# Kernel tuning notes

Hardware: AMD Instinct MI355X
Metric: run time of the kernel (lower is better)

Reference implementation:

```python
import jax, jax.numpy as jnp
import numpy as np

OT_REG = 0.1
OT_ITERS = 10
LN_EPS = 1e-5


def layernorm(x, g, b):
    m = jnp.mean(x, axis=-1, keepdims=True)
    v = jnp.mean((x - m) ** 2, axis=-1, keepdims=True)
    return (x - m) * jax.lax.rsqrt(v + LN_EPS) * g + b


def sinkhorn(C, epsilon, iters):
    # standard Sinkhorn: kernel exp(C/eps), alternate row/col normalization
    Q = jnp.exp(C / epsilon)  # [Na,B,La,Lb]
    def body(_, Q):
        Q = Q / jnp.sum(Q, axis=-1, keepdims=True)
        Q = Q / jnp.sum(Q, axis=-2, keepdims=True)
        return Q
    return jax.lax.fori_loop(0, iters, body, Q)


def setup_inputs() -> dict:
    key = jax.random.key(0)
    ks = jax.random.split(key, 16)
    Na, La, B, Lb, Din, H = 32, 32, 64, 32, 768, 768
    s = 0.02
    return {
        "entity_cls": jax.random.normal(ks[0], (Na, Din), jnp.float32),
        "entity_tokens": jax.random.normal(ks[1], (Na, La, Din), jnp.float32),
        "mention_cls": jax.random.normal(ks[2], (B, Din), jnp.float32),
        "mention_tokens": jax.random.normal(ks[3], (B, Lb, Din), jnp.float32),
        "Wq": jax.random.normal(ks[4], (Din, H), jnp.float32) * s,
        "bq": jnp.zeros((H,), jnp.float32),
        "Wk": jax.random.normal(ks[5], (Din, H), jnp.float32) * s,
        "bk": jnp.zeros((H,), jnp.float32),
        "Wv": jax.random.normal(ks[6], (Din, H), jnp.float32) * s,
        "bv": jnp.zeros((H,), jnp.float32),
        "ln1_g": jnp.ones((H,), jnp.float32),
        "ln1_b": jnp.zeros((H,), jnp.float32),
        "Wcls": jax.random.normal(ks[7], (Din, H), jnp.float32) * s,
        "bcls": jnp.zeros((H,), jnp.float32),
        "Wsp": jax.random.normal(ks[8], (H, 1), jnp.float32) * s,
        "bsp": jnp.zeros((1,), jnp.float32),
        "ln2_g": jnp.ones((H,), jnp.float32),
        "ln2_b": jnp.zeros((H,), jnp.float32),
    }


def reference(entity_cls, entity_tokens, mention_cls, mention_tokens,
              Wq, bq, Wk, bk, Wv, bv, ln1_g, ln1_b,
              Wcls, bcls, Wsp, bsp, ln2_g, ln2_b):
    # projections
    q = entity_tokens @ Wq + bq      # [Na,La,H]
    k = mention_tokens @ Wk + bk     # [B,Lb,H]
    v = mention_tokens @ Wv + bv     # [B,Lb,H]

    # cross-batch cosine similarity: [Na,B,La,Lb]
    qn = q / jnp.maximum(jnp.linalg.norm(q, axis=-1, keepdims=True), 1e-8)
    kn = k / jnp.maximum(jnp.linalg.norm(k, axis=-1, keepdims=True), 1e-8)
    C = jnp.einsum('aid,bjd->abij', qn, kn)

    # Sinkhorn on detached cost (torch uses C.detach())
    T = sinkhorn(jax.lax.stop_gradient(C), OT_REG, OT_ITERS)
    # F.normalize(dim=-1): L2 normalize last dim
    T = T / jnp.maximum(jnp.linalg.norm(T, axis=-1, keepdims=True), 1e-12)

    # attention + residual + layernorm: [Na,B,La,H]
    attended = jnp.einsum('abij,bjd->abid', T, v) + q[:, None, :, :]
    attended = layernorm(attended, ln1_g, ln1_b)

    # softpool over token dim (-2)
    w = jax.nn.softmax(attended @ Wsp + bsp, axis=-2)   # [Na,B,La,1]
    pooled = jnp.sum(attended * w, axis=-2)             # [Na,B,H]
    context = layernorm(pooled, ln2_g, ln2_b)

    # matching scores
    ecls = entity_cls @ Wcls + bcls                     # [Na,H]
    g2l = jnp.sum(ecls[:, None, :] * context, axis=-1)  # [Na,B]
    g2l = g2l.T                                         # [B,Na]
    g2g = mention_cls @ entity_cls.T                    # [B,Na]
    return (g2l + g2g) * 0.5
```

## Files before the change

### kernel.cpp

```cpp
#include <hip/hip_runtime.h>
#include <math.h>


typedef __attribute__((ext_vector_type(8))) short bfrag8;
typedef __attribute__((ext_vector_type(4))) float f32x4;

__device__ __forceinline__ unsigned short f2bf(float x) {
  union { float f; unsigned u; } v; v.f = x;
  unsigned r = v.u + 0x7fffu + ((v.u >> 16) & 1u);
  return (unsigned short)(r >> 16);
}

__global__ __launch_bounds__(256) void prep_kernel(
    const float* __restrict__ a0, const float* __restrict__ a1, const float* __restrict__ a2,
    unsigned short* __restrict__ o0, unsigned short* __restrict__ o1, unsigned short* __restrict__ o2,
    float* __restrict__ nrm,
    const float* __restrict__ W0, const float* __restrict__ W1,
    const float* __restrict__ W2, const float* __restrict__ W3,
    unsigned short* __restrict__ T0, unsigned short* __restrict__ T1,
    unsigned short* __restrict__ T2, unsigned short* __restrict__ T3) {
  __shared__ float t[32][33];
  int bx = blockIdx.x;
  if (bx < 2331) {
    if (bx < 2328) {
      const float* in; unsigned short* out; int i, n4;
      if (bx < 768)       { in = a0; out = o0; i = bx * 256 + threadIdx.x;          n4 = 196608; }
      else if (bx < 2304) { in = a1; out = o1; i = (bx - 768) * 256 + threadIdx.x;  n4 = 393216; }
      else                { in = a2; out = o2; i = (bx - 2304) * 256 + threadIdx.x; n4 = 6144; }
      if (i >= n4) return;
      float4 f = ((const float4*)in)[i];
      ushort4 o;
      o.x = f2bf(f.x); o.y = f2bf(f.y); o.z = f2bf(f.z); o.w = f2bf(f.w);
      ((ushort4*)out)[i] = o;
    } else {
      int i = (bx - 2328) * 256 + threadIdx.x;
      if (i < 768) ((float4*)nrm)[i] = make_float4(0.f, 0.f, 0.f, 0.f);
    }
    return;
  }
  int idx = bx - 2331;
  int z = idx / 576, r2 = idx % 576;
  int tby = r2 / 24, tbx = r2 % 24;
  const float* W = (z == 0) ? W0 : (z == 1) ? W1 : (z == 2) ? W2 : W3;
  unsigned short* O = (z == 0) ? T0 : (z == 1) ? T1 : (z == 2) ? T2 : T3;
  const int gx = tbx * 32, gy = tby * 32;
  const int tx = threadIdx.x & 31, ty = threadIdx.x >> 5;
#pragma unroll
  for (int u = 0; u < 4; ++u) {
    int row = ty + u * 8;
    t[row][tx] = W[(size_t)(gy + row) * 768 + gx + tx];
  }
  __syncthreads();
#pragma unroll
  for (int u = 0; u < 4; ++u) {
    int row = ty + u * 8;
    O[(size_t)(gx + row) * 768 + gy + tx] = f2bf(t[tx][row]);
  }
}

__global__ __launch_bounds__(256) void proj_gemm_kernel(
    const unsigned short* __restrict__ Ae, const unsigned short* __restrict__ Am,
    const unsigned short* __restrict__ Acls,
    const unsigned short* __restrict__ WqT, const unsigned short* __restrict__ WkT,
    const unsigned short* __restrict__ WvT, const unsigned short* __restrict__ WclsT,
    const float* __restrict__ bq, const float* __restrict__ bk,
    const float* __restrict__ bv, const float* __restrict__ bcls,
    unsigned short* __restrict__ qb, unsigned short* __restrict__ qT,
    unsigned short* __restrict__ kb, unsigned short* __restrict__ vT,
    float* __restrict__ ecls, float* __restrict__ iq_sq, float* __restrict__ ik_sq) {
  const int z = blockIdx.z;
  const int M = (z == 0) ? 1024 : (z == 3) ? 32 : 2048;
  const int bm = blockIdx.y * 128;
  if (bm >= M) return;
  const unsigned short* A = (z == 3) ? Acls : (z == 0) ? Ae : Am;
  const unsigned short* B = (z == 0) ? WqT : (z == 1) ? WkT : (z == 2) ? WvT : WclsT;
  const float* bias = (z == 0) ? bq : (z == 1) ? bk : (z == 2) ? bv : bcls;

  __shared__ unsigned short As[128 * 64];
  __shared__ unsigned short Bs[128 * 64];
  const int t = threadIdx.x;
  const int bn = blockIdx.x * 128;
  const int l = t & 63, w = t >> 6;
  const int wm = w & 1, wn = w >> 1;

  f32x4 acc[4][4];
#pragma unroll
  for (int mi = 0; mi < 4; ++mi)
#pragma unroll
    for (int nj = 0; nj < 4; ++nj) { f32x4 zz = {0.f, 0.f, 0.f, 0.f}; acc[mi][nj] = zz; }

  for (int k0 = 0; k0 < 768; k0 += 64) {
    __syncthreads();
#pragma unroll
    for (int u = 0; u < 4; ++u) {
      int c = t + u * 256;
      int row = c >> 3, kc = c & 7;
      int gm = bm + row; gm = gm < M ? gm : M - 1;
      int4 av = *(const int4*)(A + (size_t)gm * 768 + k0 + kc * 8);
      *(int4*)(As + row * 64 + ((kc ^ (row & 7)) * 8)) = av;
      int4 bv4 = *(const int4*)(B + (size_t)(bn + row) * 768 + k0 + kc * 8);
      *(int4*)(Bs + row * 64 + ((kc ^ (row & 7)) * 8)) = bv4;
    }
    __syncthreads();
#pragma unroll
    for (int kk = 0; kk < 2; ++kk) {
      bfrag8 af[4], bf[4];
      const int kc = kk * 4 + (l >> 4);
#pragma unroll
      for (int mi = 0; mi < 4; ++mi) {
        int arow = wm * 64 + mi * 16 + (l & 15);
        af[mi] = *(const bfrag8*)(As + arow * 64 + ((kc ^ (arow & 7)) * 8));
      }
#pragma unroll
      for (int nj = 0; nj < 4; ++nj) {
        int brow = wn * 64 + nj * 16 + (l & 15);
        bf[nj] = *(const bfrag8*)(Bs + brow * 64 + ((kc ^ (brow & 7)) * 8));
      }
#pragma unroll
      for (int mi = 0; mi < 4; ++mi)
#pragma unroll
        for (int nj = 0; nj < 4; ++nj)
          acc[mi][nj] = __builtin_amdgcn_mfma_f32_16x16x32_bf16(af[mi], bf[nj], acc[mi][nj], 0, 0, 0);
    }
  }

  const int col = l & 15, rq = l >> 4;
  float p[4][4] = {};
#pragma unroll
  for (int mi = 0; mi < 4; ++mi) {
#pragma unroll
    for (int nj = 0; nj < 4; ++nj) {
      int gn = bn + wn * 64 + nj * 16 + col;
      float bs = bias[gn];
#pragma unroll
      for (int r = 0; r < 4; ++r) {
        int gm = bm + wm * 64 + mi * 16 + rq * 4 + r;
        if (gm >= M) continue;
        float val = acc[mi][nj][r] + bs;
        if (z < 2) p[mi][r] += val * val;
        unsigned short bfv = f2bf(val);
        if (z == 0) {
          qb[(size_t)gm * 768 + gn] = bfv;
          int at = gm >> 5, j = gm & 31;
          qT[((size_t)at * 768 + gn) * 32 + j] = bfv;
        } else if (z == 1) kb[(size_t)gm * 768 + gn] = bfv;
        else if (z == 2) {
          int bb = gm >> 5, j = gm & 31;
          vT[((size_t)bb * 768 + gn) * 32 + j] = bfv;
        } else ecls[(size_t)gm * 768 + gn] = val;
      }
    }
  }
  if (z < 2) {
    float* nrm = (z == 0) ? iq_sq : ik_sq;
#pragma unroll
    for (int mi = 0; mi < 4; ++mi)
#pragma unroll
      for (int r = 0; r < 4; ++r) {
        float s = p[mi][r];
        s += __shfl_xor(s, 1); s += __shfl_xor(s, 2);
        s += __shfl_xor(s, 4); s += __shfl_xor(s, 8);
        if (col == 0) {
          int gm = bm + wm * 64 + mi * 16 + rq * 4 + r;
          atomicAdd(&nrm[gm], s);
        }
      }
  }
}

__global__ __launch_bounds__(512, 2) void cos_attn_kernel(
    const unsigned short* __restrict__ qb, const unsigned short* __restrict__ kb,
    const float* __restrict__ iq_sq, const float* __restrict__ ik_sq,
    const unsigned short* __restrict__ qT,
    const unsigned short* __restrict__ vT,
    const float* __restrict__ ln1_g, const float* __restrict__ ln1_b,
    const float* __restrict__ Wsp, const float* __restrict__ bsp,
    const float* __restrict__ ln2_g, const float* __restrict__ ln2_b,
    const float* __restrict__ ecls,
    const float* __restrict__ entity_cls, const float* __restrict__ mention_cls,
    float* __restrict__ out) {
  __shared__ unsigned short vLds[2 * 768 * 32];
  __shared__ __align__(16) unsigned short scratch[12288];
  __shared__ float gabLds[4 * 768];
  __shared__ float gwLds[768];
  __shared__ float ldsIq[128], ldsIk[64];
  __shared__ float red[80];

  unsigned short* As = scratch;
  unsigned short* Bs = scratch + 8192;
  unsigned short* Tlds = scratch;

  const int t = threadIdx.x;
  const int l = t & 63, w = t >> 6;
  const int bm = blockIdx.y * 128, bn = blockIdx.x * 64;
  const int wm = w & 3, wn = w >> 2;
  const int cg = l & 15, rq = l >> 4;

  {
    float sgw = 0.f, sbw = 0.f, sga[4] = {}, sba[4] = {};
    for (int h = t; h < 768; h += 512) {
      float g1 = ln1_g[h], b1 = ln1_b[h], wsp = Wsp[h];
      float g2 = ln2_g[h], b2 = ln2_b[h];
      float gw = g1 * wsp;
      gwLds[h] = gw;
      sgw += gw; sbw += b1 * wsp;
#pragma unroll
      for (int aa = 0; aa < 4; ++aa) {
        float ec = ecls[(size_t)((blockIdx.y << 2) + aa) * 768 + h];
        float gab = g2 * ec;
        gabLds[aa * 768 + h] = gab;
        sga[aa] += gab; sba[aa] += b2 * ec;
      }
    }
#pragma unroll
    for (int m = 1; m < 64; m <<= 1) {
      sgw += __shfl_xor(sgw, m); sbw += __shfl_xor(sbw, m);
#pragma unroll
      for (int aa = 0; aa < 4; ++aa) { sga[aa] += __shfl_xor(sga[aa], m); sba[aa] += __shfl_xor(sba[aa], m); }
    }
    if (l == 0) {
      red[w * 10 + 0] = sgw; red[w * 10 + 1] = sbw;
#pragma unroll
      for (int aa = 0; aa < 4; ++aa) { red[w * 10 + 2 + aa] = sga[aa]; red[w * 10 + 6 + aa] = sba[aa]; }
    }
  }
  if (t < 128) ldsIq[t] = iq_sq[bm + t];
  else if (t < 192) ldsIk[t - 128] = ik_sq[bn + t - 128];

  const int4* vsrc = (const int4*)(vT + (size_t)(blockIdx.x * 2) * 768 * 32);
  int4* vdst = (int4*)vLds;

  f32x4 acc[2][2];
#pragma unroll
  for (int mi = 0; mi < 2; ++mi)
#pragma unroll
    for (int nj = 0; nj < 2; ++nj) { f32x4 zz = {0.f, 0.f, 0.f, 0.f}; acc[mi][nj] = zz; }

  for (int k0 = 0, s = 0; k0 < 768; k0 += 64, ++s) {
    __syncthreads();
#pragma unroll
    for (int u = 0; u < 2; ++u) {
      int c = t + u * 512;
      int row = c >> 3, kc = c & 7;
      int4 av = *(const int4*)(qb + (size_t)(bm + row) * 768 + k0 + kc * 8);
      *(int4*)(As + row * 64 + ((kc ^ (row & 7)) * 8)) = av;
    }
    {
      int row = t >> 3, kc = t & 7;
      int4 bv4 = *(const int4*)(kb + (size_t)(bn + row) * 768 + k0 + kc * 8);
      *(int4*)(Bs + row * 64 + ((kc ^ (row & 7)) * 8)) = bv4;
    }
    vdst[t + s * 512] = vsrc[t + s * 512];
    __syncthreads();
#pragma unroll
    for (int kk = 0; kk < 2; ++kk) {
      bfrag8 af[2], bf[2];
      const int kc = kk * 4 + rq;
#pragma unroll
      for (int mi = 0; mi < 2; ++mi) {
        int arow = wm * 32 + mi * 16 + cg;
        af[mi] = *(const bfrag8*)(As + arow * 64 + ((kc ^ (arow & 7)) * 8));
      }
#pragma unroll
      for (int nj = 0; nj < 2; ++nj) {
        int brow = wn * 32 + nj * 16 + cg;
        bf[nj] = *(const bfrag8*)(Bs + brow * 64 + ((kc ^ (brow & 7)) * 8));
      }
#pragma unroll
      for (int mi = 0; mi < 2; ++mi)
#pragma unroll
        for (int nj = 0; nj < 2; ++nj)
          acc[mi][nj] = __builtin_amdgcn_mfma_f32_16x16x32_bf16(af[mi], bf[nj], acc[mi][nj], 0, 0, 0);
    }
  }

  float irow[2][4], icol[2];
#pragma unroll
  for (int mi = 0; mi < 2; ++mi)
#pragma unroll
    for (int r = 0; r < 4; ++r) {
      float sv = ldsIq[wm * 32 + mi * 16 + rq * 4 + r];
      irow[mi][r] = 1.0f / fmaxf(sqrtf(sv), 1e-8f);
    }
#pragma unroll
  for (int nj = 0; nj < 2; ++nj) {
    float sv = ldsIk[wn * 32 + nj * 16 + cg];
    icol[nj] = 1.0f / fmaxf(sqrtf(sv), 1e-8f);
  }
#pragma unroll
  for (int mi = 0; mi < 2; ++mi)
#pragma unroll
    for (int nj = 0; nj < 2; ++nj)
#pragma unroll
      for (int r = 0; r < 4; ++r)
        acc[mi][nj][r] = __expf(acc[mi][nj][r] * irow[mi][r] * icol[nj] * 10.0f);

  for (int it = 0; it < 10; ++it) {
#pragma unroll
    for (int mi = 0; mi < 2; ++mi)
#pragma unroll
      for (int r = 0; r < 4; ++r) {
        float rs = acc[mi][0][r] + acc[mi][1][r];
        rs += __shfl_xor(rs, 1); rs += __shfl_xor(rs, 2);
        rs += __shfl_xor(rs, 4); rs += __shfl_xor(rs, 8);
        float rinv = __builtin_amdgcn_rcpf(rs);
        acc[mi][0][r] *= rinv; acc[mi][1][r] *= rinv;
      }
#pragma unroll
    for (int nj = 0; nj < 2; ++nj) {
      float cs = acc[0][nj][0] + acc[0][nj][1] + acc[0][nj][2] + acc[0][nj][3]
               + acc[1][nj][0] + acc[1][nj][1] + acc[1][nj][2] + acc[1][nj][3];
      cs += __shfl_xor(cs, 16); cs += __shfl_xor(cs, 32);
      float cinv = __builtin_amdgcn_rcpf(cs);
#pragma unroll
      for (int mi = 0; mi < 2; ++mi)
#pragma unroll
        for (int r = 0; r < 4; ++r) acc[mi][nj][r] *= cinv;
    }
  }

#pragma unroll
  for (int mi = 0; mi < 2; ++mi)
#pragma unroll
    for (int r = 0; r < 4; ++r) {
      float ss = acc[mi][0][r] * acc[mi][0][r] + acc[mi][1][r] * acc[mi][1][r];
      ss += __shfl_xor(ss, 1); ss += __shfl_xor(ss, 2);
      ss += __shfl_xor(ss, 4); ss += __shfl_xor(ss, 8);
      float tinv = 1.0f / fmaxf(sqrtf(ss), 1e-12f);
      acc[mi][0][r] *= tinv; acc[mi][1][r] *= tinv;
    }

  __syncthreads();
  {
    unsigned short* base = Tlds + ((wn * 4 + wm) << 10);
#pragma unroll
    for (int mi = 0; mi < 2; ++mi)
#pragma unroll
      for (int nj = 0; nj < 2; ++nj)
#pragma unroll
        for (int r = 0; r < 4; ++r)
          base[(mi * 16 + rq * 4 + r) * 32 + nj * 16 + cg] = f2bf(acc[mi][nj][r]);
  }
  __syncthreads();

  const int bl = w & 1, ah = w >> 1;
  const int b_g = (blockIdx.x << 1) + bl;
  const int a_g = (blockIdx.y << 2) + ah;
  const unsigned short* vbase = vLds + bl * 24576;

  float sgw_f = 0.f, sbw_f = 0.f, sga_f = 0.f, sba_f = 0.f;
#pragma unroll
  for (int wv = 0; wv < 8; ++wv) {
    sgw_f += red[wv * 10 + 0]; sbw_f += red[wv * 10 + 1];
    sga_f += red[wv * 10 + 2 + ah]; sba_f += red[wv * 10 + 6 + ah];
  }
  sbw_f += bsp[0];

  const unsigned short* qTa = qT + (size_t)a_g * 24576;
  const unsigned short* Tp = Tlds + ((bl * 4 + ah) << 10);
  bfrag8 af[2], afI[2];
#pragma unroll
  for (int mi = 0; mi < 2; ++mi) {
    af[mi] = *(const bfrag8*)(Tp + (mi * 16 + cg) * 32 + rq * 8);
    int row = mi * 16 + cg;
    bfrag8 fI;
#pragma unroll
    for (int u = 0; u < 8; ++u) fI[u] = (row == rq * 8 + u) ? (short)0x3F80 : (short)0;
    afI[mi] = fI;
  }

  float s1[2][4] = {}, s2[2][4] = {}, a1[2][4] = {};
#pragma unroll 2
  for (int nj = 0; nj < 48; ++nj) {
    int h = nj * 16 + cg;
    bfrag8 vf = *(const bfrag8*)(vbase + h * 32 + rq * 8);
    bfrag8 qf = *(const bfrag8*)(qTa + (size_t)h * 32 + rq * 8);
    float gw = gwLds[h];
#pragma unroll
    for (int mi = 0; mi < 2; ++mi) {
      f32x4 zz = {0.f, 0.f, 0.f, 0.f};
      f32x4 p = __builtin_amdgcn_mfma_f32_16x16x32_bf16(af[mi], vf, zz, 0, 0, 0);
      f32x4 x4 = __builtin_amdgcn_mfma_f32_16x16x32_bf16(afI[mi], qf, p, 0, 0, 0);
#pragma unroll
      for (int r = 0; r < 4; ++r) {
        float x = x4[r];
        s1[mi][r] += x; s2[mi][r] += x * x; a1[mi][r] += x * gw;
      }
    }
  }
#pragma unroll
  for (int m = 1; m < 16; m <<= 1)
#pragma unroll
    for (int mi = 0; mi < 2; ++mi)
#pragma unroll
      for (int r = 0; r < 4; ++r) {
        s1[mi][r] += __shfl_xor(s1[mi][r], m);
        s2[mi][r] += __shfl_xor(s2[mi][r], m);
        a1[mi][r] += __shfl_xor(a1[mi][r], m);
      }

  float uu[2][4], c0;
  {
    float mean[2][4], rstd[2][4], logit[2][4];
#pragma unroll
    for (int mi = 0; mi < 2; ++mi)
#pragma unroll
      for (int r = 0; r < 4; ++r) {
        float m1 = s1[mi][r] * (1.0f / 768.0f);
        float var = s2[mi][r] * (1.0f / 768.0f) - m1 * m1;
        float rs = rsqrtf(var + 1e-5f);
        mean[mi][r] = m1; rstd[mi][r] = rs;
        logit[mi][r] = rs * (a1[mi][r] - m1 * sgw_f) + sbw_f;
      }
    float mx = logit[0][0];
#pragma unroll
    for (int mi = 0; mi < 2; ++mi)
#pragma unroll
      for (int r = 0; r < 4; ++r) mx = fmaxf(mx, logit[mi][r]);
    mx = fmaxf(mx, __shfl_xor(mx, 16)); mx = fmaxf(mx, __shfl_xor(mx, 32));
    float se = 0.f, ee[2][4];
#pragma unroll
    for (int mi = 0; mi < 2; ++mi)
#pragma unroll
      for (int r = 0; r < 4; ++r) { ee[mi][r] = __expf(logit[mi][r] - mx); se += ee[mi][r]; }
    se += __shfl_xor(se, 16); se += __shfl_xor(se, 32);
    const float sinv = __builtin_amdgcn_rcpf(se);
    float c0a = 0.f;
#pragma unroll
    for (int mi = 0; mi < 2; ++mi)
#pragma unroll
      for (int r = 0; r < 4; ++r) {
        uu[mi][r] = ee[mi][r] * sinv * rstd[mi][r];
        c0a += uu[mi][r] * mean[mi][r];
      }
    c0a += __shfl_xor(c0a, 16); c0a += __shfl_xor(c0a, 32);
    c0 = c0a;
  }

  float ps = 0.f, pq = 0.f, spc = 0.f;
#pragma unroll 2
  for (int nj = 0; nj < 48; ++nj) {
    int h = nj * 16 + cg;
    bfrag8 vf = *(const bfrag8*)(vbase + h * 32 + rq * 8);
    bfrag8 qf = *(const bfrag8*)(qTa + (size_t)h * 32 + rq * 8);
    float pp = 0.f;
#pragma unroll
    for (int mi = 0; mi < 2; ++mi) {
      f32x4 zz = {0.f, 0.f, 0.f, 0.f};
      f32x4 p = __builtin_amdgcn_mfma_f32_16x16x32_bf16(af[mi], vf, zz, 0, 0, 0);
      f32x4 x4 = __builtin_amdgcn_mfma_f32_16x16x32_bf16(afI[mi], qf, p, 0, 0, 0);
#pragma unroll
      for (int r = 0; r < 4; ++r) pp += uu[mi][r] * x4[r];
    }
    pp += __shfl_xor(pp, 16); pp += __shfl_xor(pp, 32);
    float pooled = ln1_g[h] * (pp - c0) + ln1_b[h];
    ps += pooled; pq += pooled * pooled;
    spc += pooled * gabLds[ah * 768 + h];
  }
#pragma unroll
  for (int m = 1; m < 16; m <<= 1) {
    ps += __shfl_xor(ps, m); pq += __shfl_xor(pq, m); spc += __shfl_xor(spc, m);
  }
  const float m2 = ps * (1.0f / 768.0f);
  const float var2 = pq * (1.0f / 768.0f) - m2 * m2;
  const float rs2 = rsqrtf(var2 + 1e-5f);
  const float* ea = entity_cls + (size_t)a_g * 768;
  const float* mb = mention_cls + (size_t)b_g * 768;
  float sg = 0.f;
#pragma unroll
  for (int u = 0; u < 12; ++u) sg += mb[l * 12 + u] * ea[l * 12 + u];
#pragma unroll
  for (int m = 1; m < 64; m <<= 1) sg += __shfl_xor(sg, m);
  float tot = rs2 * (spc - m2 * sga_f) + sba_f + sg;
  if (l == 0) out[b_g * 32 + a_g] = 0.5f * tot;
}

extern "C" void kernel_launch(void* const* d_in, const int* in_sizes, int n_in,
                              void* d_out, int out_size, void* d_ws, size_t ws_size,
                              hipStream_t stream) {
  const float* entity_cls     = (const float*)d_in[0];
  const float* entity_tokens  = (const float*)d_in[1];
  const float* mention_cls    = (const float*)d_in[2];
  const float* mention_tokens = (const float*)d_in[3];
  const float* Wq = (const float*)d_in[4];   const float* bq = (const float*)d_in[5];
  const float* Wk = (const float*)d_in[6];   const float* bk = (const float*)d_in[7];
  const float* Wv = (const float*)d_in[8];   const float* bv = (const float*)d_in[9];
  const float* ln1_g = (const float*)d_in[10]; const float* ln1_b = (const float*)d_in[11];
  const float* Wcls = (const float*)d_in[12];  const float* bcls = (const float*)d_in[13];
  const float* Wsp = (const float*)d_in[14];   const float* bsp = (const float*)d_in[15];
  const float* ln2_g = (const float*)d_in[16]; const float* ln2_b = (const float*)d_in[17];
  float* out = (float*)d_out;

  float* ws     = (float*)d_ws;
  float* ecls   = ws;
  float* iq_sq  = ecls + 24576;
  float* ik_sq  = iq_sq + 1024;
  unsigned short* qb = (unsigned short*)(ws + 55168);
  unsigned short* qT = qb + 786432;
  unsigned short* kb = qT + 786432;
  unsigned short* vT = kb + 1572864;
  char* R = (char*)(vT + 1572864);
  unsigned short* Ae    = (unsigned short*)R;
  unsigned short* Am    = Ae + 786432;
  unsigned short* Acls  = Am + 1572864;
  unsigned short* WqT   = Acls + 24576;
  unsigned short* WkT   = WqT + 589824;
  unsigned short* WvT   = WkT + 589824;
  unsigned short* WclsT = WvT + 589824;

  dim3 blk(256);
  prep_kernel<<<dim3(4635), blk, 0, stream>>>(
      entity_tokens, mention_tokens, entity_cls, Ae, Am, Acls, iq_sq,
      Wq, Wk, Wv, Wcls, WqT, WkT, WvT, WclsT);
  proj_gemm_kernel<<<dim3(6, 16, 4), blk, 0, stream>>>(
      Ae, Am, Acls, WqT, WkT, WvT, WclsT, bq, bk, bv, bcls,
      qb, qT, kb, vT, ecls, iq_sq, ik_sq);
  cos_attn_kernel<<<dim3(32, 8), dim3(512), 0, stream>>>(
      qb, kb, iq_sq, ik_sq, qT, vT,
      ln1_g, ln1_b, Wsp, bsp, ln2_g, ln2_b,
      ecls, entity_cls, mention_cls, out);
}
```

Measured before the change: 179.3 us.

## Use DPP row reductions, 512-thread projection GEMM blocks, deeper unroll in attention loops

Replaces the 16-lane shuffle-xor reduction chains with a DPP-based sum16 helper (quad permutes plus row shifts) throughout the projection and attention kernels. The projection GEMM moves from 256 to 512 threads per block, so each wave holds a 32x64 tile with half the accumulators, which is meant to improve latency hiding and occupancy. The two 48-step h loops in the attention kernel are unrolled by 4 instead of 2. The risks are DPP row-shift semantics (bound_ctrl zero fill must still give a correct full-row sum in lane 0 and elsewhere as needed) and higher register pressure from the deeper unroll.

```diff
diff --git a/kernel.cpp b/kernel.cpp
--- a/kernel.cpp
+++ b/kernel.cpp
@@ -9,6 +9,21 @@
   union { float f; unsigned u; } v; v.f = x;
   unsigned r = v.u + 0x7fffu + ((v.u >> 16) & 1u);
   return (unsigned short)(r >> 16);
+}
+
+template <int CTRL>
+__device__ __forceinline__ float dpp_add(float x) {
+  union { float f; int i; } a, b;
+  a.f = x;
+  b.i = __builtin_amdgcn_update_dpp(0, a.i, CTRL, 0xf, 0xf, true);
+  return x + b.f;
+}
+__device__ __forceinline__ float sum16(float x) {
+  x = dpp_add<0xB1>(x);
+  x = dpp_add<0x4E>(x);
+  x = dpp_add<0x124>(x);
+  x = dpp_add<0x128>(x);
+  return x;
 }
 
 __global__ __launch_bounds__(256) void prep_kernel(
@@ -58,7 +73,7 @@
   }
 }
 
-__global__ __launch_bounds__(256) void proj_gemm_kernel(
+__global__ __launch_bounds__(512, 2) void proj_gemm_kernel(
     const unsigned short* __restrict__ Ae, const unsigned short* __restrict__ Am,
     const unsigned short* __restrict__ Acls,
     const unsigned short* __restrict__ WqT, const unsigned short* __restrict__ WkT,
@@ -81,19 +96,20 @@
   const int t = threadIdx.x;
   const int bn = blockIdx.x * 128;
   const int l = t & 63, w = t >> 6;
-  const int wm = w & 1, wn = w >> 1;
-
-  f32x4 acc[4][4];
-#pragma unroll
-  for (int mi = 0; mi < 4; ++mi)
+  const int wm = w & 3, wn = w >> 2;
+  const int cg = l & 15, rq = l >> 4;
+
+  f32x4 acc[2][4];
+#pragma unroll
+  for (int mi = 0; mi < 2; ++mi)
 #pragma unroll
     for (int nj = 0; nj < 4; ++nj) { f32x4 zz = {0.f, 0.f, 0.f, 0.f}; acc[mi][nj] = zz; }
 
   for (int k0 = 0; k0 < 768; k0 += 64) {
     __syncthreads();
 #pragma unroll
-    for (int u = 0; u < 4; ++u) {
-      int c = t + u * 256;
+    for (int u = 0; u < 2; ++u) {
+      int c = t + u * 512;
       int row = c >> 3, kc = c & 7;
       int gm = bm + row; gm = gm < M ? gm : M - 1;
       int4 av = *(const int4*)(A + (size_t)gm * 768 + k0 + kc * 8);
@@ -104,37 +120,36 @@
     __syncthreads();
 #pragma unroll
     for (int kk = 0; kk < 2; ++kk) {
-      bfrag8 af[4], bf[4];
-      const int kc = kk * 4 + (l >> 4);
-#pragma unroll
-      for (int mi = 0; mi < 4; ++mi) {
-        int arow = wm * 64 + mi * 16 + (l & 15);
+      bfrag8 af[2], bf[4];
+      const int kc = kk * 4 + rq;
+#pragma unroll
+      for (int mi = 0; mi < 2; ++mi) {
+        int arow = wm * 32 + mi * 16 + cg;
         af[mi] = *(const bfrag8*)(As + arow * 64 + ((kc ^ (arow & 7)) * 8));
       }
 #pragma unroll
       for (int nj = 0; nj < 4; ++nj) {
-        int brow = wn * 64 + nj * 16 + (l & 15);
+        int brow = wn * 64 + nj * 16 + cg;
         bf[nj] = *(const bfrag8*)(Bs + brow * 64 + ((kc ^ (brow & 7)) * 8));
       }
 #pragma unroll
-      for (int mi = 0; mi < 4; ++mi)
+      for (int mi = 0; mi < 2; ++mi)
 #pragma unroll
         for (int nj = 0; nj < 4; ++nj)
           acc[mi][nj] = __builtin_amdgcn_mfma_f32_16x16x32_bf16(af[mi], bf[nj], acc[mi][nj], 0, 0, 0);
     }
   }
 
-  const int col = l & 15, rq = l >> 4;
-  float p[4][4] = {};
-#pragma unroll
-  for (int mi = 0; mi < 4; ++mi) {
+  float p[2][4] = {};
+#pragma unroll
+  for (int mi = 0; mi < 2; ++mi) {
 #pragma unroll
     for (int nj = 0; nj < 4; ++nj) {
-      int gn = bn + wn * 64 + nj * 16 + col;
+      int gn = bn + wn * 64 + nj * 16 + cg;
       float bs = bias[gn];
 #pragma unroll
       for (int r = 0; r < 4; ++r) {
-        int gm = bm + wm * 64 + mi * 16 + rq * 4 + r;
+        int gm = bm + wm * 32 + mi * 16 + rq * 4 + r;
         if (gm >= M) continue;
         float val = acc[mi][nj][r] + bs;
         if (z < 2) p[mi][r] += val * val;
@@ -154,14 +169,12 @@
   if (z < 2) {
     float* nrm = (z == 0) ? iq_sq : ik_sq;
 #pragma unroll
-    for (int mi = 0; mi < 4; ++mi)
+    for (int mi = 0; mi < 2; ++mi)
 #pragma unroll
       for (int r = 0; r < 4; ++r) {
-        float s = p[mi][r];
-        s += __shfl_xor(s, 1); s += __shfl_xor(s, 2);
-        s += __shfl_xor(s, 4); s += __shfl_xor(s, 8);
-        if (col == 0) {
-          int gm = bm + wm * 64 + mi * 16 + rq * 4 + r;
+        float s = sum16(p[mi][r]);
+        if (cg == 0) {
+          int gm = bm + wm * 32 + mi * 16 + rq * 4 + r;
           atomicAdd(&nrm[gm], s);
         }
       }
@@ -212,8 +225,11 @@
         sga[aa] += gab; sba[aa] += b2 * ec;
       }
     }
-#pragma unroll
-    for (int m = 1; m < 64; m <<= 1) {
+    sgw = sum16(sgw); sbw = sum16(sbw);
+#pragma unroll
+    for (int aa = 0; aa < 4; ++aa) { sga[aa] = sum16(sga[aa]); sba[aa] = sum16(sba[aa]); }
+#pragma unroll
+    for (int m = 16; m < 64; m <<= 1) {
       sgw += __shfl_xor(sgw, m); sbw += __shfl_xor(sbw, m);
 #pragma unroll
       for (int aa = 0; aa < 4; ++aa) { sga[aa] += __shfl_xor(sga[aa], m); sba[aa] += __shfl_xor(sba[aa], m); }
@@ -300,9 +316,7 @@
     for (int mi = 0; mi < 2; ++mi)
 #pragma unroll
       for (int r = 0; r < 4; ++r) {
-        float rs = acc[mi][0][r] + acc[mi][1][r];
-        rs += __shfl_xor(rs, 1); rs += __shfl_xor(rs, 2);
-        rs += __shfl_xor(rs, 4); rs += __shfl_xor(rs, 8);
+        float rs = sum16(acc[mi][0][r] + acc[mi][1][r]);
         float rinv = __builtin_amdgcn_rcpf(rs);
         acc[mi][0][r] *= rinv; acc[mi][1][r] *= rinv;
       }
@@ -323,9 +337,7 @@
   for (int mi = 0; mi < 2; ++mi)
 #pragma unroll
     for (int r = 0; r < 4; ++r) {
-      float ss = acc[mi][0][r] * acc[mi][0][r] + acc[mi][1][r] * acc[mi][1][r];
-      ss += __shfl_xor(ss, 1); ss += __shfl_xor(ss, 2);
-      ss += __shfl_xor(ss, 4); ss += __shfl_xor(ss, 8);
+      float ss = sum16(acc[mi][0][r] * acc[mi][0][r] + acc[mi][1][r] * acc[mi][1][r]);
       float tinv = 1.0f / fmaxf(sqrtf(ss), 1e-12f);
       acc[mi][0][r] *= tinv; acc[mi][1][r] *= tinv;
     }
@@ -370,7 +382,7 @@
   }
 
   float s1[2][4] = {}, s2[2][4] = {}, a1[2][4] = {};
-#pragma unroll 2
+#pragma unroll 4
   for (int nj = 0; nj < 48; ++nj) {
     int h = nj * 16 + cg;
     bfrag8 vf = *(const bfrag8*)(vbase + h * 32 + rq * 8);
@@ -389,15 +401,13 @@
     }
   }
 #pragma unroll
-  for (int m = 1; m < 16; m <<= 1)
-#pragma unroll
-    for (int mi = 0; mi < 2; ++mi)
-#pragma unroll
-      for (int r = 0; r < 4; ++r) {
-        s1[mi][r] += __shfl_xor(s1[mi][r], m);
-        s2[mi][r] += __shfl_xor(s2[mi][r], m);
-        a1[mi][r] += __shfl_xor(a1[mi][r], m);
-      }
+  for (int mi = 0; mi < 2; ++mi)
+#pragma unroll
+    for (int r = 0; r < 4; ++r) {
+      s1[mi][r] = sum16(s1[mi][r]);
+      s2[mi][r] = sum16(s2[mi][r]);
+      a1[mi][r] = sum16(a1[mi][r]);
+    }
 
   float uu[2][4], c0;
   {
@@ -438,7 +448,7 @@
   }
 
   float ps = 0.f, pq = 0.f, spc = 0.f;
-#pragma unroll 2
+#pragma unroll 4
   for (int nj = 0; nj < 48; ++nj) {
     int h = nj * 16 + cg;
     bfrag8 vf = *(const bfrag8*)(vbase + h * 32 + rq * 8);
@@ -457,10 +467,7 @@
     ps += pooled; pq += pooled * pooled;
     spc += pooled * gabLds[ah * 768 + h];
   }
-#pragma unroll
-  for (int m = 1; m < 16; m <<= 1) {
-    ps += __shfl_xor(ps, m); pq += __shfl_xor(pq, m); spc += __shfl_xor(spc, m);
-  }
+  ps = sum16(ps); pq = sum16(pq); spc = sum16(spc);
   const float m2 = ps * (1.0f / 768.0f);
   const float var2 = pq * (1.0f / 768.0f) - m2 * m2;
   const float rs2 = rsqrtf(var2 + 1e-5f);
@@ -469,8 +476,8 @@
   float sg = 0.f;
 #pragma unroll
   for (int u = 0; u < 12; ++u) sg += mb[l * 12 + u] * ea[l * 12 + u];
-#pragma unroll
-  for (int m = 1; m < 64; m <<= 1) sg += __shfl_xor(sg, m);
+  sg = sum16(sg);
+  sg += __shfl_xor(sg, 16); sg += __shfl_xor(sg, 32);
   float tot = rs2 * (spc - m2 * sga_f) + sba_f + sg;
   if (l == 0) out[b_g * 32 + a_g] = 0.5f * tot;
 }
@@ -508,11 +515,10 @@
   unsigned short* WvT   = WkT + 589824;
   unsigned short* WclsT = WvT + 589824;
 
-  dim3 blk(256);
-  prep_kernel<<<dim3(4635), blk, 0, stream>>>(
+  prep_kernel<<<dim3(4635), dim3(256), 0, stream>>>(
       entity_tokens, mention_tokens, entity_cls, Ae, Am, Acls, iq_sq,
       Wq, Wk, Wv, Wcls, WqT, WkT, WvT, WclsT);
-  proj_gemm_kernel<<<dim3(6, 16, 4), blk, 0, stream>>>(
+  proj_gemm_kernel<<<dim3(6, 16, 4), dim3(512), 0, stream>>>(
       Ae, Am, Acls, WqT, WkT, WvT, WclsT, bq, bk, bv, bcls,
       qb, qT, kb, vT, ecls, iq_sq, ik_sq);
   cos_attn_kernel<<<dim3(32, 8), dim3(512), 0, stream>>>(
```

New measurement: 166.1 us. -7.4%, faster.
